# Kernel tuning notes

Measured on AMD Instinct MI355X. Metric: run time of the kernel, lower is better.

The kernel has to match this reference:

```python
import jax, jax.numpy as jnp
import numpy as np

HEADS = 8


def setup_inputs() -> dict:
    key = jax.random.key(0)
    ks = jax.random.split(key, 7)
    B, C, H, W = 8, 512, 64, 64
    K, MEM = 64, 512
    s = 0.02
    return {
        "x": jax.random.normal(ks[0], (B, C, H, W), dtype=jnp.float32),
        "Ft": jax.random.normal(ks[1], (B, K, MEM), dtype=jnp.float32),
        "Wq": jax.random.normal(ks[2], (C, C), dtype=jnp.float32) * s,
        "Wk": jax.random.normal(ks[3], (C, MEM), dtype=jnp.float32) * s,
        "Wv": jax.random.normal(ks[4], (C, MEM), dtype=jnp.float32) * s,
        "Wp": jax.random.normal(ks[5], (C, C), dtype=jnp.float32) * s,
        "bp": jax.random.normal(ks[6], (C,), dtype=jnp.float32) * s,
    }


def reference(x, Ft, Wq, Wk, Wv, Wp, bp):
    B, C, H, W = x.shape
    h = HEADS
    d = C // h
    N = H * W
    # 1x1 conv query projection: (out_c, in_c) applied over spatial dims
    q = jnp.einsum('oc,bchw->bohw', Wq, x).reshape(B, h, d, N)
    q = jnp.transpose(q, (0, 1, 3, 2))                      # [B,h,N,d]
    # Linear K/V on memory tokens: Ft [B,K,MEM] @ W^T -> [B,K,C]
    k = (Ft @ Wk.T).reshape(B, -1, h, d).transpose(0, 2, 1, 3)  # [B,h,K,d]
    v = (Ft @ Wv.T).reshape(B, -1, h, d).transpose(0, 2, 1, 3)  # [B,h,K,d]
    attn = jnp.einsum('bhnc,bhkc->bhnk', q, k) / jnp.sqrt(jnp.float32(d))
    attn = jax.nn.softmax(attn, axis=-1)
    out = jnp.einsum('bhnk,bhkc->bhnc', attn, v)            # [B,h,N,d]
    out = jnp.transpose(out, (0, 1, 3, 2)).reshape(B, C, H, W)
    out = jnp.einsum('oc,bchw->bohw', Wp, out) + bp[None, :, None, None]
    return x + out
```

## Files before the change

### kernel.cpp

```cpp
#include <hip/hip_runtime.h>
#include <cstdint>
#include <cstddef>

#define BATCH 8
#define CDIM  512
#define NPIX  4096
#define NHEAD 8
#define DH    64
#define KTOK  64
#define MEM   512

typedef __attribute__((ext_vector_type(8))) short          bf8;
typedef __attribute__((ext_vector_type(4))) float          f4;
typedef __attribute__((ext_vector_type(4))) unsigned short us4;

__device__ __forceinline__ unsigned short f2bf(float f){
  union { float f; unsigned int u; } x; x.f = f;
  unsigned int r = (x.u + 0x7fffu + ((x.u >> 16) & 1u)) >> 16;
  return (unsigned short)r;
}

__device__ __forceinline__ void gld_lds16(const unsigned short* g, unsigned short* lds){
  __builtin_amdgcn_global_load_lds((const __attribute__((address_space(1))) unsigned int*)g,
                                   (__attribute__((address_space(3))) unsigned int*)lds, 16, 0, 0);
}

__global__ __launch_bounds__(256) void wconv(const float* __restrict__ wq, const float* __restrict__ wp,
                                             unsigned short* __restrict__ wqb, unsigned short* __restrict__ wpb){
  int i = (blockIdx.x * 256 + threadIdx.x) * 4;
  float4 a = *(const float4*)(wq + i);
  us4 pa = { f2bf(a.x), f2bf(a.y), f2bf(a.z), f2bf(a.w) };
  *(us4*)(wqb + i) = pa;
  float4 b = *(const float4*)(wp + i);
  us4 pb = { f2bf(b.x), f2bf(b.y), f2bf(b.z), f2bf(b.w) };
  *(us4*)(wpb + i) = pb;
}

__global__ __launch_bounds__(256) void xtrans(const float* __restrict__ x, unsigned short* __restrict__ xb){
  __shared__ __align__(16) unsigned short t[64 * 68];
  int tid = threadIdx.x;
  int n0 = blockIdx.x * 64, c0 = blockIdx.y * 64, b = blockIdx.z;
  const float* xp = x + ((size_t)(b * CDIM + c0)) * NPIX + n0;
#pragma unroll
  for (int it = 0; it < 4; ++it){
    int idx = it * 1024 + tid * 4;
    int cc = idx >> 6, nn = idx & 63;
    float4 v = *(const float4*)(xp + (size_t)cc * NPIX + nn);
    us4 pk = { f2bf(v.x), f2bf(v.y), f2bf(v.z), f2bf(v.w) };
    *(us4*)&t[cc * 68 + nn] = pk;
  }
  __syncthreads();
  unsigned short* op = xb + ((size_t)(b * NPIX + n0)) * CDIM + c0;
#pragma unroll
  for (int it = 0; it < 4; ++it){
    int idx = it * 1024 + tid * 4;
    int nn = idx >> 6, c4 = idx & 63;
    us4 pk = { t[(c4 + 0) * 68 + nn], t[(c4 + 1) * 68 + nn],
               t[(c4 + 2) * 68 + nn], t[(c4 + 3) * 68 + nn] };
    *(us4*)(op + (size_t)nn * CDIM + c4) = pk;
  }
}

__global__ __launch_bounds__(256) void kvproj(const float* __restrict__ Ft, const float* __restrict__ Wk,
                                              const float* __restrict__ Wv, unsigned short* __restrict__ kb,
                                              unsigned short* __restrict__ vt){
  __shared__ float ft[8][MEM];
  int tid = threadIdx.x;
  int cg = blockIdx.x, kk0 = blockIdx.y * 8, b = blockIdx.z;
  const float* fp = Ft + ((size_t)(b * KTOK + kk0)) * MEM;
#pragma unroll
  for (int it = 0; it < 4; ++it){
    int idx = it * 1024 + tid * 4;
    int row = idx >> 9, m = idx & 511;
    *(float4*)&ft[row][m] = *(const float4*)(fp + (size_t)row * MEM + m);
  }
  __syncthreads();
  int kv = tid >> 7, cl = tid & 127;
  int c = cg * 128 + cl;
  const float* wrow = (kv ? Wv : Wk) + (size_t)c * MEM;
  float acc[8] = {0.f,0.f,0.f,0.f,0.f,0.f,0.f,0.f};
  for (int m = 0; m < MEM; m += 4){
    float4 wv4 = *(const float4*)(wrow + m);
#pragma unroll
    for (int kk = 0; kk < 8; ++kk){
      acc[kk] += wv4.x * ft[kk][m] + wv4.y * ft[kk][m+1] + wv4.z * ft[kk][m+2] + wv4.w * ft[kk][m+3];
    }
  }
  int h = c >> 6, dd = c & 63;
  if (kv == 0){
#pragma unroll
    for (int kk = 0; kk < 8; ++kk)
      kb[(((size_t)(b * NHEAD + h)) * KTOK + kk0 + kk) * DH + dd] = f2bf(acc[kk] * 0.125f);
  } else {
#pragma unroll
    for (int kk = 0; kk < 8; ++kk)
      vt[(((size_t)(b * NHEAD + h)) * DH + dd) * KTOK + kk0 + kk] = f2bf(acc[kk]);
  }
}

#define GEMM_PRE(APTR, BPTR)                                                              \
  const int arow = l >> 3;                                                                \
  const int achk = (l & 7) ^ arow;                                                        \
  const unsigned short* aS = (APTR) + (size_t)(o0 + w * 8 + arow) * CDIM + achk * 8;      \
  const unsigned short* bS = (BPTR) + ((size_t)(b * NPIX) + n0 + w * 8 + arow) * CDIM + achk * 8;

#define STAGE(kc)                                                                         \
  {                                                                                       \
    _Pragma("unroll")                                                                     \
    for (int j = 0; j < 4; ++j){                                                          \
      gld_lds16(aS + (size_t)j * 32 * CDIM + (kc), &ab[(w + j * 4) * 512]);               \
      gld_lds16(bS + (size_t)j * 32 * CDIM + (kc), &ab[8192 + (w + j * 4) * 512]);        \
    }                                                                                     \
  }

#define GEMM_STEP(ACC)                                                                    \
  _Pragma("unroll")                                                                       \
  for (int ks = 0; ks < 2; ++ks){                                                         \
    bf8 af[4], bfr[4];                                                                    \
    _Pragma("unroll")                                                                     \
    for (int fi = 0; fi < 4; ++fi){                                                       \
      int r = ol + fi * 16 + lo;                                                          \
      af[fi] = *(const bf8*)&ab[r * 64 + (((ks * 4 + hi) ^ (r & 7)) << 3)];               \
    }                                                                                     \
    _Pragma("unroll")                                                                     \
    for (int fj = 0; fj < 4; ++fj){                                                       \
      int r = nl + fj * 16 + lo;                                                          \
      bfr[fj] = *(const bf8*)&ab[8192 + r * 64 + (((ks * 4 + hi) ^ (r & 7)) << 3)];       \
    }                                                                                     \
    _Pragma("unroll")                                                                     \
    for (int fi = 0; fi < 4; ++fi)                                                        \
      _Pragma("unroll")                                                                   \
      for (int fj = 0; fj < 4; ++fj)                                                      \
        ACC[fi][fj] = __builtin_amdgcn_mfma_f32_16x16x32_bf16(af[fi], bfr[fj], ACC[fi][fj], 0, 0, 0); \
  }

__global__ __launch_bounds__(256, 4) void qgemm(const unsigned short* __restrict__ wqb,
                                                const unsigned short* __restrict__ xb,
                                                unsigned short* __restrict__ qb){
  __shared__ __align__(16) unsigned short ab[16384];
  int tid = threadIdx.x;
  int w = tid >> 6, l = tid & 63;
  int lo = l & 15, hi = l >> 4;
  int n0 = blockIdx.x * 128, o0 = blockIdx.y * 128, b = blockIdx.z;
  int ol = (w >> 1) * 64, nl = (w & 1) * 64;

  f4 z = {0.f, 0.f, 0.f, 0.f};
  f4 acc[4][4];
#pragma unroll
  for (int i = 0; i < 4; ++i)
#pragma unroll
    for (int j = 0; j < 4; ++j) acc[i][j] = z;

  GEMM_PRE(wqb, xb)

  for (int t = 0; t < 8; ++t){
    STAGE(t * 64)
    __syncthreads();
    GEMM_STEP(acc)
    __syncthreads();
  }

  unsigned short* op = qb + ((size_t)(b * NPIX) + n0 + nl) * CDIM + o0 + ol;
#pragma unroll
  for (int fi = 0; fi < 4; ++fi)
#pragma unroll
    for (int fj = 0; fj < 4; ++fj){
      f4 v = acc[fi][fj];
      us4 pk = { f2bf(v[0]), f2bf(v[1]), f2bf(v[2]), f2bf(v[3]) };
      *(us4*)(op + (size_t)(fj * 16 + lo) * CDIM + fi * 16 + hi * 4) = pk;
    }
}

__global__ __launch_bounds__(256, 4) void attn(const unsigned short* __restrict__ qb,
                                               const unsigned short* __restrict__ kb,
                                               const unsigned short* __restrict__ vt,
                                               unsigned short* __restrict__ att){
  __shared__ __align__(16) unsigned short pb[16384];
  int tid = threadIdx.x;
  int w = tid >> 6, l = tid & 63;
  int lo = l & 15, hi = l >> 4;
  int n0 = blockIdx.x * 256 + w * 64;
  int head = blockIdx.y, b = blockIdx.z;

  const unsigned short* qh = qb + ((size_t)(b * NPIX) + n0) * CDIM + head * 64;
  const unsigned short* kh = kb + (size_t)(b * NHEAD + head) * (KTOK * DH);
  const unsigned short* vh = vt + (size_t)(b * NHEAD + head) * (DH * KTOK);
  unsigned short* P = &pb[w * 4096];

  f4 z = {0.f, 0.f, 0.f, 0.f};
  f4 accs[4][4];
#pragma unroll
  for (int i = 0; i < 4; ++i)
#pragma unroll
    for (int j = 0; j < 4; ++j) accs[i][j] = z;
#pragma unroll
  for (int ks = 0; ks < 2; ++ks){
    bf8 ka[4];
#pragma unroll
    for (int fi = 0; fi < 4; ++fi)
      ka[fi] = *(const bf8*)(kh + (fi * 16 + lo) * 64 + ks * 32 + hi * 8);
#pragma unroll
    for (int fj = 0; fj < 4; ++fj){
      bf8 qf = *(const bf8*)(qh + (size_t)(fj * 16 + lo) * CDIM + ks * 32 + hi * 8);
#pragma unroll
      for (int fi = 0; fi < 4; ++fi)
        accs[fi][fj] = __builtin_amdgcn_mfma_f32_16x16x32_bf16(ka[fi], qf, accs[fi][fj], 0, 0, 0);
    }
  }

#pragma unroll
  for (int fj = 0; fj < 4; ++fj){
    float mx = accs[0][fj][0];
#pragma unroll
    for (int fi = 0; fi < 4; ++fi)
#pragma unroll
      for (int r = 0; r < 4; ++r) mx = fmaxf(mx, accs[fi][fj][r]);
    mx = fmaxf(mx, __shfl_xor(mx, 16));
    mx = fmaxf(mx, __shfl_xor(mx, 32));
    float sm = 0.f;
#pragma unroll
    for (int fi = 0; fi < 4; ++fi)
#pragma unroll
      for (int r = 0; r < 4; ++r){
        float e = __expf(accs[fi][fj][r] - mx);
        accs[fi][fj][r] = e; sm += e;
      }
    sm += __shfl_xor(sm, 16);
    sm += __shfl_xor(sm, 32);
    float inv = 1.0f / sm;
#pragma unroll
    for (int fi = 0; fi < 4; ++fi){
      us4 pk = { f2bf(accs[fi][fj][0] * inv), f2bf(accs[fi][fj][1] * inv),
                 f2bf(accs[fi][fj][2] * inv), f2bf(accs[fi][fj][3] * inv) };
      int row = fj * 16 + lo;
      int col = fi * 16 + hi * 4;
      int cs  = (((col >> 3) ^ (row & 7)) << 3) | (col & 7);
      *(us4*)&P[row * 64 + cs] = pk;
    }
  }

  f4 acco[4][4];
#pragma unroll
  for (int i = 0; i < 4; ++i)
#pragma unroll
    for (int j = 0; j < 4; ++j) acco[i][j] = z;
#pragma unroll
  for (int ks = 0; ks < 2; ++ks){
    int sw = (((ks * 4 + hi) ^ (lo & 7)) << 3);
    bf8 va[4];
#pragma unroll
    for (int fi = 0; fi < 4; ++fi)
      va[fi] = *(const bf8*)(vh + (fi * 16 + lo) * 64 + ks * 32 + hi * 8);
#pragma unroll
    for (int fj = 0; fj < 4; ++fj){
      bf8 pf = *(const bf8*)&P[(fj * 16 + lo) * 64 + sw];
#pragma unroll
      for (int fi = 0; fi < 4; ++fi)
        acco[fi][fj] = __builtin_amdgcn_mfma_f32_16x16x32_bf16(va[fi], pf, acco[fi][fj], 0, 0, 0);
    }
  }

  unsigned short* op = att + ((size_t)(b * NPIX) + n0) * CDIM + head * 64;
#pragma unroll
  for (int fi = 0; fi < 4; ++fi)
#pragma unroll
    for (int fj = 0; fj < 4; ++fj){
      f4 v = acco[fi][fj];
      us4 pk = { f2bf(v[0]), f2bf(v[1]), f2bf(v[2]), f2bf(v[3]) };
      *(us4*)(op + (size_t)(fj * 16 + lo) * CDIM + fi * 16 + hi * 4) = pk;
    }
}

__global__ __launch_bounds__(256, 4) void pproj(const unsigned short* __restrict__ wpb,
                                                const unsigned short* __restrict__ att,
                                                const float* __restrict__ x,
                                                const float* __restrict__ bpv,
                                                float* __restrict__ out){
  __shared__ __align__(16) unsigned short ab[16384];
  int tid = threadIdx.x;
  int w = tid >> 6, l = tid & 63;
  int lo = l & 15, hi = l >> 4;
  int n0 = blockIdx.x * 128, o0 = blockIdx.y * 128, b = blockIdx.z;
  int ol = (w >> 1) * 64, nl = (w & 1) * 64;

  f4 z = {0.f, 0.f, 0.f, 0.f};
  f4 acc[4][4];
#pragma unroll
  for (int i = 0; i < 4; ++i)
#pragma unroll
    for (int j = 0; j < 4; ++j) acc[i][j] = z;

  GEMM_PRE(wpb, att)

  for (int t = 0; t < 8; ++t){
    STAGE(t * 64)
    __syncthreads();
    GEMM_STEP(acc)
    __syncthreads();
  }

#pragma unroll
  for (int fi = 0; fi < 4; ++fi)
#pragma unroll
    for (int fj = 0; fj < 4; ++fj){
      int o = o0 + ol + fi * 16 + hi * 4;
      int n = n0 + nl + fj * 16 + lo;
#pragma unroll
      for (int r = 0; r < 4; ++r){
        size_t idx = ((size_t)(b * CDIM + o + r)) * NPIX + n;
        out[idx] = acc[fi][fj][r] + bpv[o + r] + x[idx];
      }
    }
}

extern "C" void kernel_launch(void* const* d_in, const int* in_sizes, int n_in,
                              void* d_out, int out_size, void* d_ws, size_t ws_size,
                              hipStream_t stream){
  const float* x  = (const float*)d_in[0];
  const float* Ft = (const float*)d_in[1];
  const float* Wq = (const float*)d_in[2];
  const float* Wk = (const float*)d_in[3];
  const float* Wv = (const float*)d_in[4];
  const float* Wp = (const float*)d_in[5];
  const float* bp = (const float*)d_in[6];
  float* out = (float*)d_out;

  char* ws = (char*)d_ws;
  unsigned short* wqb = (unsigned short*)(ws);
  unsigned short* wpb = (unsigned short*)(ws + 524288);
  unsigned short* xb  = (unsigned short*)(ws + 1048576);
  unsigned short* qb  = (unsigned short*)(ws + 1048576 + 33554432);
  unsigned short* kb  = (unsigned short*)(ws + 1048576 + 2ull * 33554432);
  unsigned short* vt  = (unsigned short*)(ws + 1048576 + 2ull * 33554432 + 524288);

  wconv<<<dim3(256), dim3(256), 0, stream>>>(Wq, Wp, wqb, wpb);
  xtrans<<<dim3(64, 8, 8), dim3(256), 0, stream>>>(x, xb);
  kvproj<<<dim3(4, 8, 8), dim3(256), 0, stream>>>(Ft, Wk, Wv, kb, vt);
  qgemm<<<dim3(32, 4, 8), dim3(256), 0, stream>>>(wqb, xb, qb);
  attn<<<dim3(16, 8, 8), dim3(256), 0, stream>>>(qb, kb, vt, qb);
  pproj<<<dim3(32, 4, 8), dim3(256), 0, stream>>>(wpb, qb, x, bp, out);
}
```

Baseline: 128.6 us.

## Fuse Q projection GEMM with attention, keeping Q tiles in LDS

The separate qgemm and attn kernels are merged into one 512-thread qattn kernel. Each block computes a 128-channel by 256-pixel Q tile, which covers two heads. The tile is written as swizzled bf16 into LDS and consumed directly by the QK^T, softmax and PV stages, so the full Q tensor no longer makes a round trip through global memory. The output projection kernel is also retiled to 128x256 with 512 threads. In exchange, the larger LDS footprint and per-thread register use may lower occupancy.

```diff
diff --git a/kernel.cpp b/kernel.cpp
--- a/kernel.cpp
+++ b/kernel.cpp
@@ -99,33 +99,33 @@
 }
 
 #define GEMM_PRE(APTR, BPTR)                                                              \
-  const int arow = l >> 3;                                                                \
-  const int achk = (l & 7) ^ arow;                                                        \
-  const unsigned short* aS = (APTR) + (size_t)(o0 + w * 8 + arow) * CDIM + achk * 8;      \
-  const unsigned short* bS = (BPTR) + ((size_t)(b * NPIX) + n0 + w * 8 + arow) * CDIM + achk * 8;
-
-#define STAGE(kc)                                                                         \
+  const int lrow = l >> 3;                                                                \
+  const int lchk = (l & 7) ^ lrow;                                                        \
+  const unsigned short* aS = (APTR) + (size_t)(o0 + w * 8 + lrow) * CDIM + lchk * 8;      \
+  const unsigned short* bS = (BPTR) + ((size_t)(b * NPIX) + n0 + w * 8 + lrow) * CDIM + lchk * 8;
+
+#define STAGE(LDS, kc)                                                                    \
   {                                                                                       \
+    gld_lds16(aS + (kc),                        &(LDS)[w * 512]);                         \
+    gld_lds16(aS + (size_t)64 * CDIM + (kc),    &(LDS)[(w + 8) * 512]);                   \
     _Pragma("unroll")                                                                     \
-    for (int j = 0; j < 4; ++j){                                                          \
-      gld_lds16(aS + (size_t)j * 32 * CDIM + (kc), &ab[(w + j * 4) * 512]);               \
-      gld_lds16(bS + (size_t)j * 32 * CDIM + (kc), &ab[8192 + (w + j * 4) * 512]);        \
-    }                                                                                     \
-  }
-
-#define GEMM_STEP(ACC)                                                                    \
+    for (int j = 0; j < 4; ++j)                                                           \
+      gld_lds16(bS + (size_t)j * 64 * CDIM + (kc), &(LDS)[8192 + (w + j * 8) * 512]);     \
+  }
+
+#define GEMM_STEP(LDS, ACC)                                                               \
   _Pragma("unroll")                                                                       \
   for (int ks = 0; ks < 2; ++ks){                                                         \
     bf8 af[4], bfr[4];                                                                    \
     _Pragma("unroll")                                                                     \
     for (int fi = 0; fi < 4; ++fi){                                                       \
       int r = ol + fi * 16 + lo;                                                          \
-      af[fi] = *(const bf8*)&ab[r * 64 + (((ks * 4 + hi) ^ (r & 7)) << 3)];               \
+      af[fi] = *(const bf8*)&(LDS)[r * 64 + (((ks * 4 + hi) ^ (r & 7)) << 3)];            \
     }                                                                                     \
     _Pragma("unroll")                                                                     \
     for (int fj = 0; fj < 4; ++fj){                                                       \
       int r = nl + fj * 16 + lo;                                                          \
-      bfr[fj] = *(const bf8*)&ab[8192 + r * 64 + (((ks * 4 + hi) ^ (r & 7)) << 3)];       \
+      bfr[fj] = *(const bf8*)&(LDS)[8192 + r * 64 + (((ks * 4 + hi) ^ (r & 7)) << 3)];    \
     }                                                                                     \
     _Pragma("unroll")                                                                     \
     for (int fi = 0; fi < 4; ++fi)                                                        \
@@ -134,60 +134,49 @@
         ACC[fi][fj] = __builtin_amdgcn_mfma_f32_16x16x32_bf16(af[fi], bfr[fj], ACC[fi][fj], 0, 0, 0); \
   }
 
-__global__ __launch_bounds__(256, 4) void qgemm(const unsigned short* __restrict__ wqb,
+__global__ __launch_bounds__(512, 4) void qattn(const unsigned short* __restrict__ wqb,
                                                 const unsigned short* __restrict__ xb,
-                                                unsigned short* __restrict__ qb){
-  __shared__ __align__(16) unsigned short ab[16384];
+                                                const unsigned short* __restrict__ kb,
+                                                const unsigned short* __restrict__ vt,
+                                                unsigned short* __restrict__ att){
+  __shared__ __align__(16) unsigned short r0[32768];
   int tid = threadIdx.x;
   int w = tid >> 6, l = tid & 63;
   int lo = l & 15, hi = l >> 4;
-  int n0 = blockIdx.x * 128, o0 = blockIdx.y * 128, b = blockIdx.z;
-  int ol = (w >> 1) * 64, nl = (w & 1) * 64;
+  int n0 = blockIdx.x * 256, o0 = blockIdx.y * 128, b = blockIdx.z;
+  int ol = (w >> 2) * 64, nl = (w & 3) * 64;
 
   f4 z = {0.f, 0.f, 0.f, 0.f};
-  f4 acc[4][4];
+  f4 accq[4][4];
 #pragma unroll
   for (int i = 0; i < 4; ++i)
 #pragma unroll
-    for (int j = 0; j < 4; ++j) acc[i][j] = z;
+    for (int j = 0; j < 4; ++j) accq[i][j] = z;
 
   GEMM_PRE(wqb, xb)
 
   for (int t = 0; t < 8; ++t){
-    STAGE(t * 64)
+    STAGE(r0, t * 64)
     __syncthreads();
-    GEMM_STEP(acc)
+    GEMM_STEP(r0, accq)
     __syncthreads();
   }
 
-  unsigned short* op = qb + ((size_t)(b * NPIX) + n0 + nl) * CDIM + o0 + ol;
+  unsigned short* qt = &r0[w * 4096];
 #pragma unroll
   for (int fi = 0; fi < 4; ++fi)
 #pragma unroll
     for (int fj = 0; fj < 4; ++fj){
-      f4 v = acc[fi][fj];
+      f4 v = accq[fi][fj];
       us4 pk = { f2bf(v[0]), f2bf(v[1]), f2bf(v[2]), f2bf(v[3]) };
-      *(us4*)(op + (size_t)(fj * 16 + lo) * CDIM + fi * 16 + hi * 4) = pk;
-    }
-}
-
-__global__ __launch_bounds__(256, 4) void attn(const unsigned short* __restrict__ qb,
-                                               const unsigned short* __restrict__ kb,
-                                               const unsigned short* __restrict__ vt,
-                                               unsigned short* __restrict__ att){
-  __shared__ __align__(16) unsigned short pb[16384];
-  int tid = threadIdx.x;
-  int w = tid >> 6, l = tid & 63;
-  int lo = l & 15, hi = l >> 4;
-  int n0 = blockIdx.x * 256 + w * 64;
-  int head = blockIdx.y, b = blockIdx.z;
-
-  const unsigned short* qh = qb + ((size_t)(b * NPIX) + n0) * CDIM + head * 64;
+      int row = fj * 16 + lo;
+      int col = fi * 16 + hi * 4;
+      int cs  = (((col >> 3) ^ (row & 7)) << 3) | (col & 7);
+      *(us4*)&qt[row * 64 + cs] = pk;
+    }
+
+  int head = blockIdx.y * 2 + (w >> 2);
   const unsigned short* kh = kb + (size_t)(b * NHEAD + head) * (KTOK * DH);
-  const unsigned short* vh = vt + (size_t)(b * NHEAD + head) * (DH * KTOK);
-  unsigned short* P = &pb[w * 4096];
-
-  f4 z = {0.f, 0.f, 0.f, 0.f};
   f4 accs[4][4];
 #pragma unroll
   for (int i = 0; i < 4; ++i)
@@ -201,7 +190,7 @@
       ka[fi] = *(const bf8*)(kh + (fi * 16 + lo) * 64 + ks * 32 + hi * 8);
 #pragma unroll
     for (int fj = 0; fj < 4; ++fj){
-      bf8 qf = *(const bf8*)(qh + (size_t)(fj * 16 + lo) * CDIM + ks * 32 + hi * 8);
+      bf8 qf = *(const bf8*)&qt[(fj * 16 + lo) * 64 + (((ks * 4 + hi) ^ (lo & 7)) << 3)];
 #pragma unroll
       for (int fi = 0; fi < 4; ++fi)
         accs[fi][fj] = __builtin_amdgcn_mfma_f32_16x16x32_bf16(ka[fi], qf, accs[fi][fj], 0, 0, 0);
@@ -235,10 +224,11 @@
       int row = fj * 16 + lo;
       int col = fi * 16 + hi * 4;
       int cs  = (((col >> 3) ^ (row & 7)) << 3) | (col & 7);
-      *(us4*)&P[row * 64 + cs] = pk;
-    }
-  }
-
+      *(us4*)&qt[row * 64 + cs] = pk;
+    }
+  }
+
+  const unsigned short* vh = vt + (size_t)(b * NHEAD + head) * (DH * KTOK);
   f4 acco[4][4];
 #pragma unroll
   for (int i = 0; i < 4; ++i)
@@ -253,14 +243,14 @@
       va[fi] = *(const bf8*)(vh + (fi * 16 + lo) * 64 + ks * 32 + hi * 8);
 #pragma unroll
     for (int fj = 0; fj < 4; ++fj){
-      bf8 pf = *(const bf8*)&P[(fj * 16 + lo) * 64 + sw];
+      bf8 pf = *(const bf8*)&qt[(fj * 16 + lo) * 64 + sw];
 #pragma unroll
       for (int fi = 0; fi < 4; ++fi)
         acco[fi][fj] = __builtin_amdgcn_mfma_f32_16x16x32_bf16(va[fi], pf, acco[fi][fj], 0, 0, 0);
     }
   }
 
-  unsigned short* op = att + ((size_t)(b * NPIX) + n0) * CDIM + head * 64;
+  unsigned short* op = att + ((size_t)(b * NPIX) + n0 + nl) * CDIM + head * 64;
 #pragma unroll
   for (int fi = 0; fi < 4; ++fi)
 #pragma unroll
@@ -271,17 +261,17 @@
     }
 }
 
-__global__ __launch_bounds__(256, 4) void pproj(const unsigned short* __restrict__ wpb,
+__global__ __launch_bounds__(512, 4) void pproj(const unsigned short* __restrict__ wpb,
                                                 const unsigned short* __restrict__ att,
                                                 const float* __restrict__ x,
                                                 const float* __restrict__ bpv,
                                                 float* __restrict__ out){
-  __shared__ __align__(16) unsigned short ab[16384];
+  __shared__ __align__(16) unsigned short ab[24576];
   int tid = threadIdx.x;
   int w = tid >> 6, l = tid & 63;
   int lo = l & 15, hi = l >> 4;
-  int n0 = blockIdx.x * 128, o0 = blockIdx.y * 128, b = blockIdx.z;
-  int ol = (w >> 1) * 64, nl = (w & 1) * 64;
+  int n0 = blockIdx.x * 256, o0 = blockIdx.y * 128, b = blockIdx.z;
+  int ol = (w >> 2) * 64, nl = (w & 3) * 64;
 
   f4 z = {0.f, 0.f, 0.f, 0.f};
   f4 acc[4][4];
@@ -293,9 +283,9 @@
   GEMM_PRE(wpb, att)
 
   for (int t = 0; t < 8; ++t){
-    STAGE(t * 64)
+    STAGE(ab, t * 64)
     __syncthreads();
-    GEMM_STEP(acc)
+    GEMM_STEP(ab, acc)
     __syncthreads();
   }
 
@@ -329,14 +319,13 @@
   unsigned short* wqb = (unsigned short*)(ws);
   unsigned short* wpb = (unsigned short*)(ws + 524288);
   unsigned short* xb  = (unsigned short*)(ws + 1048576);
-  unsigned short* qb  = (unsigned short*)(ws + 1048576 + 33554432);
+  unsigned short* att = (unsigned short*)(ws + 1048576 + 33554432);
   unsigned short* kb  = (unsigned short*)(ws + 1048576 + 2ull * 33554432);
   unsigned short* vt  = (unsigned short*)(ws + 1048576 + 2ull * 33554432 + 524288);
 
   wconv<<<dim3(256), dim3(256), 0, stream>>>(Wq, Wp, wqb, wpb);
   xtrans<<<dim3(64, 8, 8), dim3(256), 0, stream>>>(x, xb);
   kvproj<<<dim3(4, 8, 8), dim3(256), 0, stream>>>(Ft, Wk, Wv, kb, vt);
-  qgemm<<<dim3(32, 4, 8), dim3(256), 0, stream>>>(wqb, xb, qb);
-  attn<<<dim3(16, 8, 8), dim3(256), 0, stream>>>(qb, kb, vt, qb);
-  pproj<<<dim3(32, 4, 8), dim3(256), 0, stream>>>(wpb, qb, x, bp, out);
-}
+  qattn<<<dim3(16, 4, 8), dim3(512), 0, stream>>>(wqb, xb, kb, vt, att);
+  pproj<<<dim3(16, 4, 8), dim3(512), 0, stream>>>(wpb, att, x, bp, out);
+}
```

New measurement: 114.3 us. 1.13x faster.
